# Kernel tuning notes

Measured on AMD Instinct MI355X. Metric: run time of the kernel, lower is better.

## Reference

```python
import jax, jax.numpy as jnp
import numpy as np

N = 50000       # nodes
E = 600000      # edges (avg degree 12)
F_IN = 64       # input_bands
F_HID = 128     # 2 * input_bands
F_OUT = 128     # output_bands
EPS = 1e-5      # BatchNorm eps


def setup_inputs() -> dict:
    key = jax.random.key(0)
    ks = jax.random.split(key, 12)
    x = jax.random.normal(ks[0], (N, F_IN), jnp.float32)
    edge_index = jax.random.randint(ks[1], (2, E), 0, N, dtype=jnp.int32)
    # GCNConv weight (glorot-ish) and bias
    W1 = jax.random.normal(ks[2], (F_IN, F_HID), jnp.float32) / np.sqrt(F_IN)
    b1 = jnp.zeros((F_HID,), jnp.float32)
    gamma1 = jnp.ones((F_HID,), jnp.float32)
    beta1 = jnp.zeros((F_HID,), jnp.float32)
    # SAGEConv: lin_l (aggregated neighbors, with bias), lin_r (root, no bias)
    Wl = jax.random.normal(ks[3], (F_HID, F_OUT), jnp.float32) / np.sqrt(F_HID)
    bl = jnp.zeros((F_OUT,), jnp.float32)
    Wr = jax.random.normal(ks[4], (F_HID, F_OUT), jnp.float32) / np.sqrt(F_HID)
    gamma2 = jnp.ones((F_OUT,), jnp.float32)
    beta2 = jnp.zeros((F_OUT,), jnp.float32)
    return {"x": x, "edge_index": edge_index, "W1": W1, "b1": b1,
            "gamma1": gamma1, "beta1": beta1, "Wl": Wl, "bl": bl,
            "Wr": Wr, "gamma2": gamma2, "beta2": beta2}


def _bn_train(h, gamma, beta):
    # BatchNorm1d in training mode: biased batch stats over the node axis
    mean = h.mean(axis=0)
    var = h.var(axis=0)
    return gamma * (h - mean) * jax.lax.rsqrt(var + EPS) + beta


def _gcn_conv(x, src, dst, W, b):
    # PyG GCNConv: x' = D^{-1/2}(A + I)D^{-1/2} X W + b
    h = x @ W                                   # [N, F_HID]
    loop = jnp.arange(N, dtype=src.dtype)
    src_sl = jnp.concatenate([src, loop])       # self-loops appended
    dst_sl = jnp.concatenate([dst, loop])
    deg = jax.ops.segment_sum(jnp.ones(E + N, h.dtype), dst_sl, num_segments=N)
    dis = jnp.where(deg > 0, jax.lax.rsqrt(deg), 0.0)  # deg^{-1/2}, inf -> 0
    norm = dis[src_sl] * dis[dst_sl]            # [E+N]
    msg = h[src_sl] * norm[:, None]             # gather + scale
    return jax.ops.segment_sum(msg, dst_sl, num_segments=N) + b


def _sage_conv(x, src, dst, Wl, bl, Wr):
    # PyG SAGEConv (mean aggr): x' = lin_l(mean_{j in N(i)} x_j) + lin_r(x_i)
    cnt = jax.ops.segment_sum(jnp.ones(E, x.dtype), dst, num_segments=N)
    neigh = jax.ops.segment_sum(x[src], dst, num_segments=N)
    neigh = neigh / jnp.maximum(cnt, 1.0)[:, None]
    return neigh @ Wl + bl + x @ Wr


def reference(x, edge_index, W1, b1, gamma1, beta1, Wl, bl, Wr, gamma2, beta2):
    src, dst = edge_index[0], edge_index[1]
    h = _gcn_conv(x, src, dst, W1, b1)
    h = jax.nn.relu(_bn_train(h, gamma1, beta1))  # dropout = identity (eval)
    h = _sage_conv(h, src, dst, Wl, bl, Wr)
    h = jax.nn.relu(_bn_train(h, gamma2, beta2))
    return h
```

## Files before the change

kernel.cpp:

```cpp
#include <hip/hip_runtime.h>


#define NN 50000
#define NE 600000
#define FIN 64
#define FHID 128
#define BN_EPS 1e-5f
#define CAP 64

typedef __attribute__((ext_vector_type(8))) short short8;
typedef __attribute__((ext_vector_type(4))) float f32x4;

__device__ __forceinline__ unsigned short f2bf(float f) {
  unsigned u = __float_as_uint(f);
  return (unsigned short)((u + 0x7FFFu + ((u >> 16) & 1u)) >> 16);
}
__device__ __forceinline__ float bfs(unsigned short u) {
  return __uint_as_float(((unsigned)u) << 16);
}
__device__ __forceinline__ float bflo(unsigned v) { return __uint_as_float(v << 16); }
__device__ __forceinline__ float bfhi(unsigned v) { return __uint_as_float(v & 0xFFFF0000u); }
__device__ __forceinline__ unsigned pk2(float lo, float hi) {
  return (unsigned)f2bf(lo) | ((unsigned)f2bf(hi) << 16);
}

__global__ __launch_bounds__(256) void bucket_fill(
    const int* __restrict__ src, const int* __restrict__ dst,
    int* __restrict__ cnt, int* __restrict__ csr,
    const float* __restrict__ W1, const float* __restrict__ Wl,
    const float* __restrict__ Wr, short* __restrict__ Wp1,
    short* __restrict__ Wp2, int nbE4) {
  int tid = threadIdx.x;
  if ((int)blockIdx.x < nbE4) {
    int e4 = blockIdx.x * 256 + tid;
    if (e4 * 4 < NE) {
      int4 d4 = ((const int4*)dst)[e4];
      int4 s4 = ((const int4*)src)[e4];
      int p;
      p = atomicAdd(&cnt[d4.x], 1); if (p < CAP) csr[(size_t)d4.x * CAP + p] = s4.x;
      p = atomicAdd(&cnt[d4.y], 1); if (p < CAP) csr[(size_t)d4.y * CAP + p] = s4.y;
      p = atomicAdd(&cnt[d4.z], 1); if (p < CAP) csr[(size_t)d4.z * CAP + p] = s4.z;
      p = atomicAdd(&cnt[d4.w], 1); if (p < CAP) csr[(size_t)d4.w * CAP + p] = s4.w;
    }
  } else {
    int widx = (blockIdx.x - nbE4) * 256 + tid;
    if (widx < 8192) {
      int kk = widx & 7, lane = (widx >> 3) & 63, ks = (widx >> 9) & 1,
          n = widx >> 10;
      int q = lane >> 4, r = lane & 15;
      int k = ks * 32 + q * 8 + kk, col = n * 16 + r;
      Wp1[widx] = (short)f2bf(W1[k * 128 + col]);
    } else if (widx < 8192 + 32768) {
      int w2 = widx - 8192;
      int kk = w2 & 7, lane = (w2 >> 3) & 63, ks = (w2 >> 9) & 7, n = w2 >> 12;
      int q = lane >> 4, r = lane & 15;
      int k = ks * 32 + q * 8 + kk, col = n * 16 + r;
      float wv = (k < 128) ? Wl[k * 128 + col] : Wr[(k - 128) * 128 + col];
      Wp2[w2] = (short)f2bf(wv);
    }
  }
}

__global__ __launch_bounds__(256) void scale_x(const float* __restrict__ x,
                                               const int* __restrict__ cnt,
                                               ushort4* __restrict__ xs,
                                               int* __restrict__ csr) {
  int i = blockIdx.x * 256 + threadIdx.x;
  float4 v = ((const float4*)x)[i];
  int node = i >> 4;
  float d = rsqrtf((float)(cnt[node] + 1));
  xs[i] = make_ushort4(f2bf(v.x * d), f2bf(v.y * d), f2bf(v.z * d), f2bf(v.w * d));
  if (i < NN) {
    int deg = min(cnt[i], CAP);
    int deg8 = (deg + 7) & ~7;
    int* cb = csr + (size_t)i * CAP;
    for (int p = deg; p < deg8; ++p) cb[p] = 0;
  }
}

__device__ __forceinline__ void gacc(float& a0, float& a1, float& a2, float& a3,
                                     ushort4 v) {
  a0 += bfs(v.x); a1 += bfs(v.y); a2 += bfs(v.z); a3 += bfs(v.w);
}

__global__ __launch_bounds__(256) void gcn_block(
    const unsigned short* __restrict__ xs, const int* __restrict__ csr,
    const int* __restrict__ cnt, const short* __restrict__ Wp1,
    const float* __restrict__ b1, unsigned short* __restrict__ hb,
    float* __restrict__ sums1, float* __restrict__ sumsq1) {
  __shared__ unsigned short xaS[64][72];
  __shared__ float lsum[128], lsq[128];
  int tid = threadIdx.x;
  if (tid < 128) { lsum[tid] = 0.f; lsq[tid] = 0.f; }
  int row_base = blockIdx.x * 64;
  int li = tid & 15, g = tid >> 4;
  ushort4 zv = *(const ushort4*)(xs + li * 4);
  for (int it = 0; it < 4; ++it) {
    int lr = g * 4 + it;
    int node = row_base + lr;
    if (node < NN) {
      int degr = cnt[node];
      int deg = min(degr, CAP);
      int deg8 = (deg + 7) & ~7;
      float di = rsqrtf((float)(degr + 1));
      ushort4 sv = *(const ushort4*)(xs + (size_t)node * FIN + li * 4);
      float a0 = bfs(sv.x), a1 = bfs(sv.y), a2 = bfs(sv.z), a3 = bfs(sv.w);
      const int* cb = csr + (size_t)node * CAP;
      int4 sA = *(const int4*)(cb);
      int4 sB = *(const int4*)(cb + 4);
      for (int e = 0; e < deg8; e += 8) {
        int pn = min(e + 8, CAP - 8);
        int4 nA = *(const int4*)(cb + pn);
        int4 nB = *(const int4*)(cb + pn + 4);
        ushort4 v0 = *(const ushort4*)(xs + (size_t)sA.x * FIN + li * 4);
        ushort4 v1 = *(const ushort4*)(xs + (size_t)sA.y * FIN + li * 4);
        ushort4 v2 = *(const ushort4*)(xs + (size_t)sA.z * FIN + li * 4);
        ushort4 v3 = *(const ushort4*)(xs + (size_t)sA.w * FIN + li * 4);
        ushort4 v4 = *(const ushort4*)(xs + (size_t)sB.x * FIN + li * 4);
        ushort4 v5 = *(const ushort4*)(xs + (size_t)sB.y * FIN + li * 4);
        ushort4 v6 = *(const ushort4*)(xs + (size_t)sB.z * FIN + li * 4);
        ushort4 v7 = *(const ushort4*)(xs + (size_t)sB.w * FIN + li * 4);
        gacc(a0, a1, a2, a3, v0); gacc(a0, a1, a2, a3, v1);
        gacc(a0, a1, a2, a3, v2); gacc(a0, a1, a2, a3, v3);
        gacc(a0, a1, a2, a3, v4); gacc(a0, a1, a2, a3, v5);
        gacc(a0, a1, a2, a3, v6); gacc(a0, a1, a2, a3, v7);
        sA = nA; sB = nB;
      }
      float pc = (float)(deg8 - deg);
      a0 -= pc * bfs(zv.x); a1 -= pc * bfs(zv.y);
      a2 -= pc * bfs(zv.z); a3 -= pc * bfs(zv.w);
      *(ushort4*)(&xaS[lr][li * 4]) = make_ushort4(
          f2bf(di * a0), f2bf(di * a1), f2bf(di * a2), f2bf(di * a3));
    }
  }
  __syncthreads();

  int lane = tid & 63, w = tid >> 6, r = lane & 15, q = lane >> 4;
  short8 af[2];
#pragma unroll
  for (int ks = 0; ks < 2; ++ks)
    af[ks] = *(const short8*)(&xaS[w * 16 + r][ks * 32 + q * 8]);
  f32x4 acc[8];
#pragma unroll
  for (int n = 0; n < 8; ++n) acc[n] = (f32x4){0.f, 0.f, 0.f, 0.f};
#pragma unroll
  for (int ks = 0; ks < 2; ++ks)
#pragma unroll
    for (int n = 0; n < 8; ++n) {
      short8 bf = *(const short8*)(Wp1 + ((size_t)(n * 2 + ks) * 64 + lane) * 8);
      acc[n] = __builtin_amdgcn_mfma_f32_16x16x32_bf16(af[ks], bf, acc[n], 0, 0, 0);
    }

  float bias_r[8];
#pragma unroll
  for (int n = 0; n < 8; ++n) bias_r[n] = b1[n * 16 + r];
  float cs[8], cq[8];
#pragma unroll
  for (int n = 0; n < 8; ++n) { cs[n] = 0.f; cq[n] = 0.f; }
#pragma unroll
  for (int i = 0; i < 4; ++i) {
    int row = row_base + w * 16 + q * 4 + i;
    if (row < NN) {
#pragma unroll
      for (int n = 0; n < 8; ++n) {
        float v = acc[n][i] + bias_r[n];
        hb[(size_t)row * 128 + n * 16 + r] = f2bf(v);
        cs[n] += v;
        cq[n] += v * v;
      }
    }
  }
#pragma unroll
  for (int n = 0; n < 8; ++n) {
    atomicAdd(&lsum[n * 16 + r], cs[n]);
    atomicAdd(&lsq[n * 16 + r], cq[n]);
  }
  __syncthreads();
  if (tid < 128) {
    atomicAdd(&sums1[tid], lsum[tid]);
    atomicAdd(&sumsq1[tid], lsq[tid]);
  }
}

__device__ __forceinline__ void sbn(float* a, uint4 v, const float* sc,
                                    const float* sh) {
  a[0] += fmaxf(fmaf(bflo(v.x), sc[0], sh[0]), 0.f);
  a[1] += fmaxf(fmaf(bfhi(v.x), sc[1], sh[1]), 0.f);
  a[2] += fmaxf(fmaf(bflo(v.y), sc[2], sh[2]), 0.f);
  a[3] += fmaxf(fmaf(bfhi(v.y), sc[3], sh[3]), 0.f);
  a[4] += fmaxf(fmaf(bflo(v.z), sc[4], sh[4]), 0.f);
  a[5] += fmaxf(fmaf(bfhi(v.z), sc[5], sh[5]), 0.f);
  a[6] += fmaxf(fmaf(bflo(v.w), sc[6], sh[6]), 0.f);
  a[7] += fmaxf(fmaf(bfhi(v.w), sc[7], sh[7]), 0.f);
}

__global__ __launch_bounds__(256) void sage_block(
    const unsigned short* __restrict__ hb, const int* __restrict__ csr,
    const int* __restrict__ cnt, const short* __restrict__ Wp2,
    const float* __restrict__ bl, const float* __restrict__ sums1,
    const float* __restrict__ sumsq1, const float* __restrict__ g1,
    const float* __restrict__ be1, float* __restrict__ out,
    float* __restrict__ sums2, float* __restrict__ sumsq2) {
  __shared__ unsigned short nbS[64][136];
  __shared__ float scB[128], shB[128], lsum[128], lsq[128];
  int tid = threadIdx.x;
  if (tid < 128) {
    lsum[tid] = 0.f; lsq[tid] = 0.f;
    float mean = sums1[tid] * (1.0f / NN);
    float var = fmaxf(sumsq1[tid] * (1.0f / NN) - mean * mean, 0.f);
    float s = g1[tid] * rsqrtf(var + BN_EPS);
    scB[tid] = s;
    shB[tid] = be1[tid] - mean * s;
  }
  __syncthreads();

  int row_base = blockIdx.x * 64;
  int li = tid & 15, g = tid >> 4;
  const unsigned* hbu = (const unsigned*)hb;
  float sc8[8], sh8[8];
#pragma unroll
  for (int j = 0; j < 8; ++j) { sc8[j] = scB[li * 8 + j]; sh8[j] = shB[li * 8 + j]; }
  float zb[8];
  {
    uint4 zr = *(const uint4*)(hbu + li * 4);
    float t[8] = {0,0,0,0,0,0,0,0};
    sbn(t, zr, sc8, sh8);
#pragma unroll
    for (int j = 0; j < 8; ++j) zb[j] = t[j];
  }
  for (int it = 0; it < 4; ++it) {
    int lr = g * 4 + it;
    int node = row_base + lr;
    if (node < NN) {
      int degr = cnt[node];
      int deg = min(degr, CAP);
      int deg8 = (deg + 7) & ~7;
      float a[8];
#pragma unroll
      for (int j = 0; j < 8; ++j) a[j] = 0.f;
      const int* cb = csr + (size_t)node * CAP;
      int4 sA = *(const int4*)(cb);
      int4 sB = *(const int4*)(cb + 4);
      for (int e = 0; e < deg8; e += 8) {
        int pn = min(e + 8, CAP - 8);
        int4 nA = *(const int4*)(cb + pn);
        int4 nB = *(const int4*)(cb + pn + 4);
        uint4 v0 = *(const uint4*)(hbu + (size_t)sA.x * 64 + li * 4);
        uint4 v1 = *(const uint4*)(hbu + (size_t)sA.y * 64 + li * 4);
        uint4 v2 = *(const uint4*)(hbu + (size_t)sA.z * 64 + li * 4);
        uint4 v3 = *(const uint4*)(hbu + (size_t)sA.w * 64 + li * 4);
        uint4 v4 = *(const uint4*)(hbu + (size_t)sB.x * 64 + li * 4);
        uint4 v5 = *(const uint4*)(hbu + (size_t)sB.y * 64 + li * 4);
        uint4 v6 = *(const uint4*)(hbu + (size_t)sB.z * 64 + li * 4);
        uint4 v7 = *(const uint4*)(hbu + (size_t)sB.w * 64 + li * 4);
        sbn(a, v0, sc8, sh8); sbn(a, v1, sc8, sh8);
        sbn(a, v2, sc8, sh8); sbn(a, v3, sc8, sh8);
        sbn(a, v4, sc8, sh8); sbn(a, v5, sc8, sh8);
        sbn(a, v6, sc8, sh8); sbn(a, v7, sc8, sh8);
        sA = nA; sB = nB;
      }
      float pc = (float)(deg8 - deg);
#pragma unroll
      for (int j = 0; j < 8; ++j) a[j] -= pc * zb[j];
      float inv = 1.0f / fmaxf((float)degr, 1.0f);
      uint4 o;
      o.x = pk2(a[0] * inv, a[1] * inv);
      o.y = pk2(a[2] * inv, a[3] * inv);
      o.z = pk2(a[4] * inv, a[5] * inv);
      o.w = pk2(a[6] * inv, a[7] * inv);
      *(uint4*)(&nbS[lr][li * 8]) = o;
    }
  }
  __syncthreads();

  int lane = tid & 63, w = tid >> 6, r = lane & 15, q = lane >> 4;
  int rowg = row_base + w * 16 + r;
  rowg = rowg < NN ? rowg : NN - 1;
  short8 af[8];
#pragma unroll
  for (int ks = 0; ks < 4; ++ks)
    af[ks] = *(const short8*)(&nbS[w * 16 + r][ks * 32 + q * 8]);
#pragma unroll
  for (int ks = 4; ks < 8; ++ks) {
    int kg = (ks - 4) * 32 + q * 8;
    short8 raw = *(const short8*)((const short*)hb + (size_t)rowg * 128 + kg);
    short8 t;
#pragma unroll
    for (int j = 0; j < 8; ++j) {
      float f = fmaxf(fmaf(bfs((unsigned short)raw[j]), scB[kg + j], shB[kg + j]), 0.f);
      t[j] = (short)f2bf(f);
    }
    af[ks] = t;
  }
  f32x4 acc[8];
#pragma unroll
  for (int n = 0; n < 8; ++n) acc[n] = (f32x4){0.f, 0.f, 0.f, 0.f};
#pragma unroll
  for (int ks = 0; ks < 8; ++ks)
#pragma unroll
    for (int n = 0; n < 8; ++n) {
      short8 bf = *(const short8*)(Wp2 + ((size_t)(n * 8 + ks) * 64 + lane) * 8);
      acc[n] = __builtin_amdgcn_mfma_f32_16x16x32_bf16(af[ks], bf, acc[n], 0, 0, 0);
    }

  float bias_r[8];
#pragma unroll
  for (int n = 0; n < 8; ++n) bias_r[n] = bl[n * 16 + r];
  float cs[8], cq[8];
#pragma unroll
  for (int n = 0; n < 8; ++n) { cs[n] = 0.f; cq[n] = 0.f; }
#pragma unroll
  for (int i = 0; i < 4; ++i) {
    int row = row_base + w * 16 + q * 4 + i;
    if (row < NN) {
#pragma unroll
      for (int n = 0; n < 8; ++n) {
        float v = acc[n][i] + bias_r[n];
        out[(size_t)row * 128 + n * 16 + r] = v;
        cs[n] += v;
        cq[n] += v * v;
      }
    }
  }
#pragma unroll
  for (int n = 0; n < 8; ++n) {
    atomicAdd(&lsum[n * 16 + r], cs[n]);
    atomicAdd(&lsq[n * 16 + r], cq[n]);
  }
  __syncthreads();
  if (tid < 128) {
    atomicAdd(&sums2[tid], lsum[tid]);
    atomicAdd(&sumsq2[tid], lsq[tid]);
  }
}

__global__ __launch_bounds__(256) void bn_apply_f32(float* __restrict__ out,
                                                    const float* __restrict__ sums,
                                                    const float* __restrict__ sumsq,
                                                    const float* __restrict__ gamma,
                                                    const float* __restrict__ beta) {
  __shared__ float sc[128], sh[128];
  int t = threadIdx.x;
  if (t < 128) {
    float mean = sums[t] * (1.0f / NN);
    float var = fmaxf(sumsq[t] * (1.0f / NN) - mean * mean, 0.f);
    float inv = rsqrtf(var + BN_EPS);
    float s = gamma[t] * inv;
    sc[t] = s;
    sh[t] = beta[t] - mean * s;
  }
  __syncthreads();
  int i4 = blockIdx.x * 256 + t;
  float4 v = ((const float4*)out)[i4];
  int f = (i4 & 31) * 4;
  v.x = fmaxf(fmaf(v.x, sc[f + 0], sh[f + 0]), 0.f);
  v.y = fmaxf(fmaf(v.y, sc[f + 1], sh[f + 1]), 0.f);
  v.z = fmaxf(fmaf(v.z, sc[f + 2], sh[f + 2]), 0.f);
  v.w = fmaxf(fmaf(v.w, sc[f + 3], sh[f + 3]), 0.f);
  ((float4*)out)[i4] = v;
}

extern "C" void kernel_launch(void* const* d_in, const int* in_sizes, int n_in,
                              void* d_out, int out_size, void* d_ws, size_t ws_size,
                              hipStream_t stream) {
  const float* x   = (const float*)d_in[0];
  const int*   ei  = (const int*)d_in[1];
  const float* W1  = (const float*)d_in[2];
  const float* b1  = (const float*)d_in[3];
  const float* g1  = (const float*)d_in[4];
  const float* be1 = (const float*)d_in[5];
  const float* Wl  = (const float*)d_in[6];
  const float* bl  = (const float*)d_in[7];
  const float* Wr  = (const float*)d_in[8];
  const float* g2  = (const float*)d_in[9];
  const float* be2 = (const float*)d_in[10];
  const int* srcp = ei;
  const int* dstp = ei + NE;

  char* w = (char*)d_ws;
  auto alloc = [&](size_t bytes) {
    char* p = w;
    w += (bytes + 255) & ~(size_t)255;
    return p;
  };
  size_t zbytes = (NN + 1024) * 4;
  char* zz = (char*)alloc(zbytes);
  int*   cnt   = (int*)zz;
  float* stats = (float*)(cnt + NN);
  float* sums1 = stats,       *sumsq1 = stats + 128;
  float* sums2 = stats + 512, *sumsq2 = stats + 640;

  int*   csr = (int*)alloc((size_t)NN * CAP * 4);
  unsigned short* xs = (unsigned short*)alloc((size_t)NN * FIN * 2);
  unsigned short* hb = (unsigned short*)alloc((size_t)NN * FHID * 2);
  short* Wp1 = (short*)alloc(8192 * 2);
  short* Wp2 = (short*)alloc(32768 * 2);

  hipMemsetAsync(zz, 0, zbytes, stream);

  int nbE4 = (NE / 4 + 255) / 256;
  int nbW  = (8192 + 32768 + 255) / 256;
  int nb64 = (NN + 63) / 64;

  bucket_fill<<<nbE4 + nbW, 256, 0, stream>>>(srcp, dstp, cnt, csr, W1, Wl, Wr,
                                              Wp1, Wp2, nbE4);
  scale_x<<<NN * FIN / 4 / 256, 256, 0, stream>>>(x, cnt, (ushort4*)xs, csr);
  gcn_block<<<nb64, 256, 0, stream>>>(xs, csr, cnt, Wp1, b1, hb, sums1, sumsq1);
  sage_block<<<nb64, 256, 0, stream>>>(hb, csr, cnt, Wp2, bl, sums1, sumsq1,
                                       g1, be1, (float*)d_out, sums2, sumsq2);
  bn_apply_f32<<<NN * FHID / 4 / 256, 256, 0, stream>>>((float*)d_out, sums2,
                                                        sumsq2, g2, be2);
}
```

Before: 245.1 us.

## Shrink GCN/SAGE blocks to 16 nodes and slot BN stat atomics

The gcn_block and sage_block kernels now handle 16 nodes per block instead of 64. Each of the 16 thread groups gathers one node, and each wave computes two output column tiles of the MFMA GEMM. This quadruples the grid to raise occupancy and latency hiding for the irregular gathers. The global BatchNorm sum atomics are also spread over 32 slots, summed by the consumer kernels, to cut atomic contention on 128 addresses. The cost is more blocks, more per-block overhead, and redundant weight loads per block, and bounds checks are dropped on the assumption that NN is divisible by 16.

Measured after the change: 220.4 us. 1.11x faster.

```diff
diff --git a/kernel.cpp b/kernel.cpp
--- a/kernel.cpp
+++ b/kernel.cpp
@@ -7,6 +7,7 @@
 #define FHID 128
 #define BN_EPS 1e-5f
 #define CAP 64
+#define NSLOT 32
 
 typedef __attribute__((ext_vector_type(8))) short short8;
 typedef __attribute__((ext_vector_type(4))) float f32x4;
@@ -87,98 +88,86 @@
     const unsigned short* __restrict__ xs, const int* __restrict__ csr,
     const int* __restrict__ cnt, const short* __restrict__ Wp1,
     const float* __restrict__ b1, unsigned short* __restrict__ hb,
-    float* __restrict__ sums1, float* __restrict__ sumsq1) {
-  __shared__ unsigned short xaS[64][72];
+    float* __restrict__ sums1s, float* __restrict__ sumsq1s) {
+  __shared__ unsigned short xaS[16][72];
   __shared__ float lsum[128], lsq[128];
   int tid = threadIdx.x;
   if (tid < 128) { lsum[tid] = 0.f; lsq[tid] = 0.f; }
-  int row_base = blockIdx.x * 64;
+  int row_base = blockIdx.x * 16;
   int li = tid & 15, g = tid >> 4;
-  ushort4 zv = *(const ushort4*)(xs + li * 4);
-  for (int it = 0; it < 4; ++it) {
-    int lr = g * 4 + it;
-    int node = row_base + lr;
-    if (node < NN) {
-      int degr = cnt[node];
-      int deg = min(degr, CAP);
-      int deg8 = (deg + 7) & ~7;
-      float di = rsqrtf((float)(degr + 1));
-      ushort4 sv = *(const ushort4*)(xs + (size_t)node * FIN + li * 4);
-      float a0 = bfs(sv.x), a1 = bfs(sv.y), a2 = bfs(sv.z), a3 = bfs(sv.w);
-      const int* cb = csr + (size_t)node * CAP;
-      int4 sA = *(const int4*)(cb);
-      int4 sB = *(const int4*)(cb + 4);
-      for (int e = 0; e < deg8; e += 8) {
-        int pn = min(e + 8, CAP - 8);
-        int4 nA = *(const int4*)(cb + pn);
-        int4 nB = *(const int4*)(cb + pn + 4);
-        ushort4 v0 = *(const ushort4*)(xs + (size_t)sA.x * FIN + li * 4);
-        ushort4 v1 = *(const ushort4*)(xs + (size_t)sA.y * FIN + li * 4);
-        ushort4 v2 = *(const ushort4*)(xs + (size_t)sA.z * FIN + li * 4);
-        ushort4 v3 = *(const ushort4*)(xs + (size_t)sA.w * FIN + li * 4);
-        ushort4 v4 = *(const ushort4*)(xs + (size_t)sB.x * FIN + li * 4);
-        ushort4 v5 = *(const ushort4*)(xs + (size_t)sB.y * FIN + li * 4);
-        ushort4 v6 = *(const ushort4*)(xs + (size_t)sB.z * FIN + li * 4);
-        ushort4 v7 = *(const ushort4*)(xs + (size_t)sB.w * FIN + li * 4);
-        gacc(a0, a1, a2, a3, v0); gacc(a0, a1, a2, a3, v1);
-        gacc(a0, a1, a2, a3, v2); gacc(a0, a1, a2, a3, v3);
-        gacc(a0, a1, a2, a3, v4); gacc(a0, a1, a2, a3, v5);
-        gacc(a0, a1, a2, a3, v6); gacc(a0, a1, a2, a3, v7);
-        sA = nA; sB = nB;
-      }
-      float pc = (float)(deg8 - deg);
-      a0 -= pc * bfs(zv.x); a1 -= pc * bfs(zv.y);
-      a2 -= pc * bfs(zv.z); a3 -= pc * bfs(zv.w);
-      *(ushort4*)(&xaS[lr][li * 4]) = make_ushort4(
-          f2bf(di * a0), f2bf(di * a1), f2bf(di * a2), f2bf(di * a3));
-    }
+  int node = row_base + g;
+  {
+    int degr = cnt[node];
+    int deg = min(degr, CAP);
+    int deg8 = (deg + 7) & ~7;
+    float di = rsqrtf((float)(degr + 1));
+    ushort4 sv = *(const ushort4*)(xs + (size_t)node * FIN + li * 4);
+    float a0 = bfs(sv.x), a1 = bfs(sv.y), a2 = bfs(sv.z), a3 = bfs(sv.w);
+    ushort4 zv = *(const ushort4*)(xs + li * 4);
+    const int* cb = csr + (size_t)node * CAP;
+    int4 sA = *(const int4*)(cb);
+    int4 sB = *(const int4*)(cb + 4);
+    for (int e = 0; e < deg8; e += 8) {
+      int pn = min(e + 8, CAP - 8);
+      int4 nA = *(const int4*)(cb + pn);
+      int4 nB = *(const int4*)(cb + pn + 4);
+      ushort4 v0 = *(const ushort4*)(xs + (size_t)sA.x * FIN + li * 4);
+      ushort4 v1 = *(const ushort4*)(xs + (size_t)sA.y * FIN + li * 4);
+      ushort4 v2 = *(const ushort4*)(xs + (size_t)sA.z * FIN + li * 4);
+      ushort4 v3 = *(const ushort4*)(xs + (size_t)sA.w * FIN + li * 4);
+      ushort4 v4 = *(const ushort4*)(xs + (size_t)sB.x * FIN + li * 4);
+      ushort4 v5 = *(const ushort4*)(xs + (size_t)sB.y * FIN + li * 4);
+      ushort4 v6 = *(const ushort4*)(xs + (size_t)sB.z * FIN + li * 4);
+      ushort4 v7 = *(const ushort4*)(xs + (size_t)sB.w * FIN + li * 4);
+      gacc(a0, a1, a2, a3, v0); gacc(a0, a1, a2, a3, v1);
+      gacc(a0, a1, a2, a3, v2); gacc(a0, a1, a2, a3, v3);
+      gacc(a0, a1, a2, a3, v4); gacc(a0, a1, a2, a3, v5);
+      gacc(a0, a1, a2, a3, v6); gacc(a0, a1, a2, a3, v7);
+      sA = nA; sB = nB;
+    }
+    float pc = (float)(deg8 - deg);
+    a0 -= pc * bfs(zv.x); a1 -= pc * bfs(zv.y);
+    a2 -= pc * bfs(zv.z); a3 -= pc * bfs(zv.w);
+    *(ushort4*)(&xaS[g][li * 4]) = make_ushort4(
+        f2bf(di * a0), f2bf(di * a1), f2bf(di * a2), f2bf(di * a3));
   }
   __syncthreads();
 
   int lane = tid & 63, w = tid >> 6, r = lane & 15, q = lane >> 4;
-  short8 af[2];
-#pragma unroll
-  for (int ks = 0; ks < 2; ++ks)
-    af[ks] = *(const short8*)(&xaS[w * 16 + r][ks * 32 + q * 8]);
-  f32x4 acc[8];
-#pragma unroll
-  for (int n = 0; n < 8; ++n) acc[n] = (f32x4){0.f, 0.f, 0.f, 0.f};
-#pragma unroll
-  for (int ks = 0; ks < 2; ++ks)
-#pragma unroll
-    for (int n = 0; n < 8; ++n) {
-      short8 bf = *(const short8*)(Wp1 + ((size_t)(n * 2 + ks) * 64 + lane) * 8);
-      acc[n] = __builtin_amdgcn_mfma_f32_16x16x32_bf16(af[ks], bf, acc[n], 0, 0, 0);
-    }
-
-  float bias_r[8];
-#pragma unroll
-  for (int n = 0; n < 8; ++n) bias_r[n] = b1[n * 16 + r];
-  float cs[8], cq[8];
-#pragma unroll
-  for (int n = 0; n < 8; ++n) { cs[n] = 0.f; cq[n] = 0.f; }
+  int n0 = w * 2, n1 = w * 2 + 1;
+  short8 af0 = *(const short8*)(&xaS[r][q * 8]);
+  short8 af1 = *(const short8*)(&xaS[r][32 + q * 8]);
+  f32x4 acc0 = (f32x4){0.f, 0.f, 0.f, 0.f}, acc1 = acc0;
+  acc0 = __builtin_amdgcn_mfma_f32_16x16x32_bf16(
+      af0, *(const short8*)(Wp1 + ((size_t)(n0 * 2 + 0) * 64 + lane) * 8), acc0, 0, 0, 0);
+  acc1 = __builtin_amdgcn_mfma_f32_16x16x32_bf16(
+      af0, *(const short8*)(Wp1 + ((size_t)(n1 * 2 + 0) * 64 + lane) * 8), acc1, 0, 0, 0);
+  acc0 = __builtin_amdgcn_mfma_f32_16x16x32_bf16(
+      af1, *(const short8*)(Wp1 + ((size_t)(n0 * 2 + 1) * 64 + lane) * 8), acc0, 0, 0, 0);
+  acc1 = __builtin_amdgcn_mfma_f32_16x16x32_bf16(
+      af1, *(const short8*)(Wp1 + ((size_t)(n1 * 2 + 1) * 64 + lane) * 8), acc1, 0, 0, 0);
+
+  float b0 = b1[n0 * 16 + r], bb1 = b1[n1 * 16 + r];
+  float cs0 = 0.f, cq0 = 0.f, cs1 = 0.f, cq1 = 0.f;
 #pragma unroll
   for (int i = 0; i < 4; ++i) {
-    int row = row_base + w * 16 + q * 4 + i;
-    if (row < NN) {
-#pragma unroll
-      for (int n = 0; n < 8; ++n) {
-        float v = acc[n][i] + bias_r[n];
-        hb[(size_t)row * 128 + n * 16 + r] = f2bf(v);
-        cs[n] += v;
-        cq[n] += v * v;
-      }
-    }
-  }
-#pragma unroll
-  for (int n = 0; n < 8; ++n) {
-    atomicAdd(&lsum[n * 16 + r], cs[n]);
-    atomicAdd(&lsq[n * 16 + r], cq[n]);
-  }
+    int row = row_base + q * 4 + i;
+    float v0 = acc0[i] + b0;
+    float v1 = acc1[i] + bb1;
+    hb[(size_t)row * 128 + n0 * 16 + r] = f2bf(v0);
+    hb[(size_t)row * 128 + n1 * 16 + r] = f2bf(v1);
+    cs0 += v0; cq0 += v0 * v0;
+    cs1 += v1; cq1 += v1 * v1;
+  }
+  atomicAdd(&lsum[n0 * 16 + r], cs0);
+  atomicAdd(&lsq[n0 * 16 + r], cq0);
+  atomicAdd(&lsum[n1 * 16 + r], cs1);
+  atomicAdd(&lsq[n1 * 16 + r], cq1);
   __syncthreads();
   if (tid < 128) {
-    atomicAdd(&sums1[tid], lsum[tid]);
-    atomicAdd(&sumsq1[tid], lsq[tid]);
+    int s = blockIdx.x & (NSLOT - 1);
+    atomicAdd(&sums1s[s * 128 + tid], lsum[tid]);
+    atomicAdd(&sumsq1s[s * 128 + tid], lsq[tid]);
   }
 }
 
@@ -197,89 +186,86 @@
 __global__ __launch_bounds__(256) void sage_block(
     const unsigned short* __restrict__ hb, const int* __restrict__ csr,
     const int* __restrict__ cnt, const short* __restrict__ Wp2,
-    const float* __restrict__ bl, const float* __restrict__ sums1,
-    const float* __restrict__ sumsq1, const float* __restrict__ g1,
+    const float* __restrict__ bl, const float* __restrict__ sums1s,
+    const float* __restrict__ sumsq1s, const float* __restrict__ g1,
     const float* __restrict__ be1, float* __restrict__ out,
-    float* __restrict__ sums2, float* __restrict__ sumsq2) {
-  __shared__ unsigned short nbS[64][136];
+    float* __restrict__ sums2s, float* __restrict__ sumsq2s) {
+  __shared__ unsigned short nbS[16][136];
   __shared__ float scB[128], shB[128], lsum[128], lsq[128];
   int tid = threadIdx.x;
   if (tid < 128) {
     lsum[tid] = 0.f; lsq[tid] = 0.f;
-    float mean = sums1[tid] * (1.0f / NN);
-    float var = fmaxf(sumsq1[tid] * (1.0f / NN) - mean * mean, 0.f);
-    float s = g1[tid] * rsqrtf(var + BN_EPS);
-    scB[tid] = s;
-    shB[tid] = be1[tid] - mean * s;
-  }
-  __syncthreads();
-
-  int row_base = blockIdx.x * 64;
+    float ms = 0.f, vs = 0.f;
+#pragma unroll
+    for (int s = 0; s < NSLOT; ++s) {
+      ms += sums1s[s * 128 + tid];
+      vs += sumsq1s[s * 128 + tid];
+    }
+    float mean = ms * (1.0f / NN);
+    float var = fmaxf(vs * (1.0f / NN) - mean * mean, 0.f);
+    float sgm = g1[tid] * rsqrtf(var + BN_EPS);
+    scB[tid] = sgm;
+    shB[tid] = be1[tid] - mean * sgm;
+  }
+  __syncthreads();
+
+  int row_base = blockIdx.x * 16;
   int li = tid & 15, g = tid >> 4;
+  int node = row_base + g;
   const unsigned* hbu = (const unsigned*)hb;
-  float sc8[8], sh8[8];
-#pragma unroll
-  for (int j = 0; j < 8; ++j) { sc8[j] = scB[li * 8 + j]; sh8[j] = shB[li * 8 + j]; }
-  float zb[8];
   {
-    uint4 zr = *(const uint4*)(hbu + li * 4);
-    float t[8] = {0,0,0,0,0,0,0,0};
-    sbn(t, zr, sc8, sh8);
-#pragma unroll
-    for (int j = 0; j < 8; ++j) zb[j] = t[j];
-  }
-  for (int it = 0; it < 4; ++it) {
-    int lr = g * 4 + it;
-    int node = row_base + lr;
-    if (node < NN) {
-      int degr = cnt[node];
-      int deg = min(degr, CAP);
-      int deg8 = (deg + 7) & ~7;
-      float a[8];
-#pragma unroll
-      for (int j = 0; j < 8; ++j) a[j] = 0.f;
-      const int* cb = csr + (size_t)node * CAP;
-      int4 sA = *(const int4*)(cb);
-      int4 sB = *(const int4*)(cb + 4);
-      for (int e = 0; e < deg8; e += 8) {
-        int pn = min(e + 8, CAP - 8);
-        int4 nA = *(const int4*)(cb + pn);
-        int4 nB = *(const int4*)(cb + pn + 4);
-        uint4 v0 = *(const uint4*)(hbu + (size_t)sA.x * 64 + li * 4);
-        uint4 v1 = *(const uint4*)(hbu + (size_t)sA.y * 64 + li * 4);
-        uint4 v2 = *(const uint4*)(hbu + (size_t)sA.z * 64 + li * 4);
-        uint4 v3 = *(const uint4*)(hbu + (size_t)sA.w * 64 + li * 4);
-        uint4 v4 = *(const uint4*)(hbu + (size_t)sB.x * 64 + li * 4);
-        uint4 v5 = *(const uint4*)(hbu + (size_t)sB.y * 64 + li * 4);
-        uint4 v6 = *(const uint4*)(hbu + (size_t)sB.z * 64 + li * 4);
-        uint4 v7 = *(const uint4*)(hbu + (size_t)sB.w * 64 + li * 4);
-        sbn(a, v0, sc8, sh8); sbn(a, v1, sc8, sh8);
-        sbn(a, v2, sc8, sh8); sbn(a, v3, sc8, sh8);
-        sbn(a, v4, sc8, sh8); sbn(a, v5, sc8, sh8);
-        sbn(a, v6, sc8, sh8); sbn(a, v7, sc8, sh8);
-        sA = nA; sB = nB;
-      }
-      float pc = (float)(deg8 - deg);
-#pragma unroll
-      for (int j = 0; j < 8; ++j) a[j] -= pc * zb[j];
-      float inv = 1.0f / fmaxf((float)degr, 1.0f);
-      uint4 o;
-      o.x = pk2(a[0] * inv, a[1] * inv);
-      o.y = pk2(a[2] * inv, a[3] * inv);
-      o.z = pk2(a[4] * inv, a[5] * inv);
-      o.w = pk2(a[6] * inv, a[7] * inv);
-      *(uint4*)(&nbS[lr][li * 8]) = o;
-    }
+    float sc8[8], sh8[8];
+#pragma unroll
+    for (int j = 0; j < 8; ++j) { sc8[j] = scB[li * 8 + j]; sh8[j] = shB[li * 8 + j]; }
+    float zb[8] = {0, 0, 0, 0, 0, 0, 0, 0};
+    sbn(zb, *(const uint4*)(hbu + li * 4), sc8, sh8);
+    int degr = cnt[node];
+    int deg = min(degr, CAP);
+    int deg8 = (deg + 7) & ~7;
+    float a[8];
+#pragma unroll
+    for (int j = 0; j < 8; ++j) a[j] = 0.f;
+    const int* cb = csr + (size_t)node * CAP;
+    int4 sA = *(const int4*)(cb);
+    int4 sB = *(const int4*)(cb + 4);
+    for (int e = 0; e < deg8; e += 8) {
+      int pn = min(e + 8, CAP - 8);
+      int4 nA = *(const int4*)(cb + pn);
+      int4 nB = *(const int4*)(cb + pn + 4);
+      uint4 v0 = *(const uint4*)(hbu + (size_t)sA.x * 64 + li * 4);
+      uint4 v1 = *(const uint4*)(hbu + (size_t)sA.y * 64 + li * 4);
+      uint4 v2 = *(const uint4*)(hbu + (size_t)sA.z * 64 + li * 4);
+      uint4 v3 = *(const uint4*)(hbu + (size_t)sA.w * 64 + li * 4);
+      uint4 v4 = *(const uint4*)(hbu + (size_t)sB.x * 64 + li * 4);
+      uint4 v5 = *(const uint4*)(hbu + (size_t)sB.y * 64 + li * 4);
+      uint4 v6 = *(const uint4*)(hbu + (size_t)sB.z * 64 + li * 4);
+      uint4 v7 = *(const uint4*)(hbu + (size_t)sB.w * 64 + li * 4);
+      sbn(a, v0, sc8, sh8); sbn(a, v1, sc8, sh8);
+      sbn(a, v2, sc8, sh8); sbn(a, v3, sc8, sh8);
+      sbn(a, v4, sc8, sh8); sbn(a, v5, sc8, sh8);
+      sbn(a, v6, sc8, sh8); sbn(a, v7, sc8, sh8);
+      sA = nA; sB = nB;
+    }
+    float pc = (float)(deg8 - deg);
+#pragma unroll
+    for (int j = 0; j < 8; ++j) a[j] -= pc * zb[j];
+    float inv = 1.0f / fmaxf((float)degr, 1.0f);
+    uint4 o;
+    o.x = pk2(a[0] * inv, a[1] * inv);
+    o.y = pk2(a[2] * inv, a[3] * inv);
+    o.z = pk2(a[4] * inv, a[5] * inv);
+    o.w = pk2(a[6] * inv, a[7] * inv);
+    *(uint4*)(&nbS[g][li * 8]) = o;
   }
   __syncthreads();
 
   int lane = tid & 63, w = tid >> 6, r = lane & 15, q = lane >> 4;
-  int rowg = row_base + w * 16 + r;
-  rowg = rowg < NN ? rowg : NN - 1;
+  int n0 = w * 2, n1 = w * 2 + 1;
   short8 af[8];
 #pragma unroll
   for (int ks = 0; ks < 4; ++ks)
-    af[ks] = *(const short8*)(&nbS[w * 16 + r][ks * 32 + q * 8]);
+    af[ks] = *(const short8*)(&nbS[r][ks * 32 + q * 8]);
+  int rowg = row_base + r;
 #pragma unroll
   for (int ks = 4; ks < 8; ++ks) {
     int kg = (ks - 4) * 32 + q * 8;
@@ -292,62 +278,61 @@
     }
     af[ks] = t;
   }
-  f32x4 acc[8];
-#pragma unroll
-  for (int n = 0; n < 8; ++n) acc[n] = (f32x4){0.f, 0.f, 0.f, 0.f};
-#pragma unroll
-  for (int ks = 0; ks < 8; ++ks)
-#pragma unroll
-    for (int n = 0; n < 8; ++n) {
-      short8 bf = *(const short8*)(Wp2 + ((size_t)(n * 8 + ks) * 64 + lane) * 8);
-      acc[n] = __builtin_amdgcn_mfma_f32_16x16x32_bf16(af[ks], bf, acc[n], 0, 0, 0);
-    }
-
-  float bias_r[8];
-#pragma unroll
-  for (int n = 0; n < 8; ++n) bias_r[n] = bl[n * 16 + r];
-  float cs[8], cq[8];
-#pragma unroll
-  for (int n = 0; n < 8; ++n) { cs[n] = 0.f; cq[n] = 0.f; }
+  f32x4 acc0 = (f32x4){0.f, 0.f, 0.f, 0.f}, acc1 = acc0;
+#pragma unroll
+  for (int ks = 0; ks < 8; ++ks) {
+    acc0 = __builtin_amdgcn_mfma_f32_16x16x32_bf16(
+        af[ks], *(const short8*)(Wp2 + ((size_t)(n0 * 8 + ks) * 64 + lane) * 8),
+        acc0, 0, 0, 0);
+    acc1 = __builtin_amdgcn_mfma_f32_16x16x32_bf16(
+        af[ks], *(const short8*)(Wp2 + ((size_t)(n1 * 8 + ks) * 64 + lane) * 8),
+        acc1, 0, 0, 0);
+  }
+
+  float b0 = bl[n0 * 16 + r], bb1 = bl[n1 * 16 + r];
+  float cs0 = 0.f, cq0 = 0.f, cs1 = 0.f, cq1 = 0.f;
 #pragma unroll
   for (int i = 0; i < 4; ++i) {
-    int row = row_base + w * 16 + q * 4 + i;
-    if (row < NN) {
-#pragma unroll
-      for (int n = 0; n < 8; ++n) {
-        float v = acc[n][i] + bias_r[n];
-        out[(size_t)row * 128 + n * 16 + r] = v;
-        cs[n] += v;
-        cq[n] += v * v;
-      }
-    }
-  }
-#pragma unroll
-  for (int n = 0; n < 8; ++n) {
-    atomicAdd(&lsum[n * 16 + r], cs[n]);
-    atomicAdd(&lsq[n * 16 + r], cq[n]);
-  }
+    int row = row_base + q * 4 + i;
+    float v0 = acc0[i] + b0;
+    float v1 = acc1[i] + bb1;
+    out[(size_t)row * 128 + n0 * 16 + r] = v0;
+    out[(size_t)row * 128 + n1 * 16 + r] = v1;
+    cs0 += v0; cq0 += v0 * v0;
+    cs1 += v1; cq1 += v1 * v1;
+  }
+  atomicAdd(&lsum[n0 * 16 + r], cs0);
+  atomicAdd(&lsq[n0 * 16 + r], cq0);
+  atomicAdd(&lsum[n1 * 16 + r], cs1);
+  atomicAdd(&lsq[n1 * 16 + r], cq1);
   __syncthreads();
   if (tid < 128) {
-    atomicAdd(&sums2[tid], lsum[tid]);
-    atomicAdd(&sumsq2[tid], lsq[tid]);
+    int s = blockIdx.x & (NSLOT - 1);
+    atomicAdd(&sums2s[s * 128 + tid], lsum[tid]);
+    atomicAdd(&sumsq2s[s * 128 + tid], lsq[tid]);
   }
 }
 
 __global__ __launch_bounds__(256) void bn_apply_f32(float* __restrict__ out,
-                                                    const float* __restrict__ sums,
-                                                    const float* __restrict__ sumsq,
+                                                    const float* __restrict__ sums2s,
+                                                    const float* __restrict__ sumsq2s,
                                                     const float* __restrict__ gamma,
                                                     const float* __restrict__ beta) {
   __shared__ float sc[128], sh[128];
   int t = threadIdx.x;
   if (t < 128) {
-    float mean = sums[t] * (1.0f / NN);
-    float var = fmaxf(sumsq[t] * (1.0f / NN) - mean * mean, 0.f);
+    float ms = 0.f, vs = 0.f;
+#pragma unroll
+    for (int s = 0; s < NSLOT; ++s) {
+      ms += sums2s[s * 128 + t];
+      vs += sumsq2s[s * 128 + t];
+    }
+    float mean = ms * (1.0f / NN);
+    float var = fmaxf(vs * (1.0f / NN) - mean * mean, 0.f);
     float inv = rsqrtf(var + BN_EPS);
-    float s = gamma[t] * inv;
-    sc[t] = s;
-    sh[t] = beta[t] - mean * s;
+    float sgm = gamma[t] * inv;
+    sc[t] = sgm;
+    sh[t] = beta[t] - mean * sgm;
   }
   __syncthreads();
   int i4 = blockIdx.x * 256 + t;
@@ -383,12 +368,12 @@
     w += (bytes + 255) & ~(size_t)255;
     return p;
   };
-  size_t zbytes = (NN + 1024) * 4;
+  size_t zbytes = ((size_t)NN + 4 * NSLOT * 128) * 4;
   char* zz = (char*)alloc(zbytes);
   int*   cnt   = (int*)zz;
   float* stats = (float*)(cnt + NN);
-  float* sums1 = stats,       *sumsq1 = stats + 128;
-  float* sums2 = stats + 512, *sumsq2 = stats + 640;
+  float* sums1s = stats,                     *sumsq1s = stats + NSLOT * 128;
+  float* sums2s = stats + 2 * NSLOT * 128,   *sumsq2s = stats + 3 * NSLOT * 128;
 
   int*   csr = (int*)alloc((size_t)NN * CAP * 4);
   unsigned short* xs = (unsigned short*)alloc((size_t)NN * FIN * 2);
@@ -400,14 +385,14 @@
 
   int nbE4 = (NE / 4 + 255) / 256;
   int nbW  = (8192 + 32768 + 255) / 256;
-  int nb64 = (NN + 63) / 64;
+  int nb16 = NN / 16;
 
   bucket_fill<<<nbE4 + nbW, 256, 0, stream>>>(srcp, dstp, cnt, csr, W1, Wl, Wr,
                                               Wp1, Wp2, nbE4);
   scale_x<<<NN * FIN / 4 / 256, 256, 0, stream>>>(x, cnt, (ushort4*)xs, csr);
-  gcn_block<<<nb64, 256, 0, stream>>>(xs, csr, cnt, Wp1, b1, hb, sums1, sumsq1);
-  sage_block<<<nb64, 256, 0, stream>>>(hb, csr, cnt, Wp2, bl, sums1, sumsq1,
-                                       g1, be1, (float*)d_out, sums2, sumsq2);
-  bn_apply_f32<<<NN * FHID / 4 / 256, 256, 0, stream>>>((float*)d_out, sums2,
-                                                        sumsq2, g2, be2);
-}
+  gcn_block<<<nb16, 256, 0, stream>>>(xs, csr, cnt, Wp1, b1, hb, sums1s, sumsq1s);
+  sage_block<<<nb16, 256, 0, stream>>>(hb, csr, cnt, Wp2, bl, sums1s, sumsq1s,
+                                       g1, be1, (float*)d_out, sums2s, sumsq2s);
+  bn_apply_f32<<<NN * FHID / 4 / 256, 256, 0, stream>>>((float*)d_out, sums2s,
+                                                        sumsq2s, g2, be2);
+}
```
